# Kernel optimization log

Hardware: AMD Instinct MI355X
Metric: run time of the kernel (lower is better)

## Reference

```python
import jax, jax.numpy as jnp
import numpy as np

N, E, F, C = 100000, 1600000, 64, 256


def setup_inputs() -> dict:
    key = jax.random.key(0)
    ks = jax.random.split(key, 9)

    def lin(k, fi, fo):
        kw, kb = jax.random.split(k)
        w = jax.random.normal(kw, (fi, fo), jnp.float32) * np.float32(1.0 / np.sqrt(fi))
        b = jax.random.normal(kb, (fo,), jnp.float32) * 0.001
        return w, b

    content = jax.random.normal(ks[0], (N, C), jnp.float32)
    node_emb = jax.random.normal(ks[1], (N + 1, F), jnp.float32) * np.float32(1.0 / (100 * F))
    proj_w, proj_b = lin(ks[2], C, F)
    c0w1, c0b1 = lin(ks[3], 2 * F, 4 * F)   # first layer: inp=2F -> 4F
    c0w2, c0b2 = lin(ks[4], 4 * F, F)
    c1w1, c1b1 = lin(ks[5], 3 * F, 6 * F)   # prediction layer: inp=3F -> 6F
    c1w2, c1b2 = lin(ks[6], 6 * F, F)
    nid = jnp.arange(N, dtype=jnp.int32)
    src = jax.random.randint(ks[7], (E,), 0, N, dtype=jnp.int32)
    dst = jax.random.randint(ks[8], (E,), 0, N, dtype=jnp.int32)
    return dict(content=content, node_emb=node_emb, proj_w=proj_w, proj_b=proj_b,
                c0w1=c0w1, c0b1=c0b1, c0w2=c0w2, c0b2=c0b2,
                c1w1=c1w1, c1b1=c1b1, c1w2=c1w2, c1b2=c1b2,
                nid=nid, src=src, dst=dst)


def _l2norm(x):
    # per-node L2 renorm with clamp(min=1e-6) like torch .norm().clamp
    n = jnp.linalg.norm(x, axis=1, keepdims=True)
    return x / jnp.maximum(n, 1e-6)


def _forward(content, node_emb, proj_w, proj_b,
             c0w1, c0b1, c0w2, c0b2, c1w1, c1b1, c1w2, c1b2,
             nid, src, dst):
    n = content.shape[0]
    lrelu = lambda x: jax.nn.leaky_relu(x, 0.1)
    # node init: embedding + projected content (GaussianNoise is identity in eval)
    h = node_emb[nid + 1] + lrelu(content @ proj_w + proj_b)
    # w = sum of 'one' over in-neighbors = in-degree
    deg = jax.ops.segment_sum(jnp.ones(src.shape[0], h.dtype), dst, num_segments=n)
    wden = jnp.maximum(deg - 1.0, 1.0)[:, None]  # (w - 1).clamp(min=1)

    # ---- layer 0 (first_layer) ----
    h_agg = jax.ops.segment_sum(h[src], dst, num_segments=n)  # copy_src('h') + sum
    h_agg = (h_agg - h) / wden
    z = lrelu(jnp.concatenate([h, h_agg], axis=1) @ c0w1 + c0b1)
    h_new = _l2norm(lrelu(z @ c0w2 + c0b2))
    h_res = _l2norm(h_agg)  # skip is None since in_dims == out_dims
    h = h_new

    # ---- layer 1 (prediction_layer) ----
    h_agg = jax.ops.segment_sum(h[src], dst, num_segments=n)
    h_res_sum = jax.ops.segment_sum(h_res[src], dst, num_segments=n)
    h_agg = (h_agg - h) / wden
    z = lrelu(jnp.concatenate([h, h_agg, h_res_sum], axis=1) @ c1w1 + c1b1)
    h_new = z @ c1w2 + c1b2  # prediction layer: no trailing LeakyReLU
    return _l2norm(h_new)


def reference(content, node_emb, proj_w, proj_b, c0w1, c0b1, c0w2, c0b2,
              c1w1, c1b1, c1w2, c1b2, nid, src, dst):
    return _forward(content, node_emb, proj_w, proj_b,
                    c0w1, c0b1, c0w2, c0b2, c1w1, c1b1, c1w2, c1b2,
                    nid, src, dst)
```

## Files before the change

### kernel.cpp

```cpp
#include <hip/hip_runtime.h>

typedef _Float16 half_t;
typedef half_t h8 __attribute__((ext_vector_type(8)));
typedef float f32x4 __attribute__((ext_vector_type(4)));
typedef unsigned int uint;

__device__ __forceinline__ float lrelu_f(float x){ return x >= 0.f ? x : 0.1f*x; }

__device__ __forceinline__ float2 unpack_h2(uint v){
  half_t lo = __builtin_bit_cast(half_t, (unsigned short)(v & 0xffffu));
  half_t hi = __builtin_bit_cast(half_t, (unsigned short)(v >> 16));
  return make_float2((float)lo, (float)hi);
}
__device__ __forceinline__ uint pack_h2(float a, float b){
  unsigned short lo = __builtin_bit_cast(unsigned short, (half_t)a);
  unsigned short hi = __builtin_bit_cast(unsigned short, (half_t)b);
  return (uint)lo | ((uint)hi << 16);
}

enum { EPI_INIT=0, EPI_LRELU=1, EPI_LRELU_L2=2, EPI_L2=3 };
constexpr int CAP = 64;

__global__ void pack_all_kernel(const float* __restrict__ s0, half_t* __restrict__ d0,
                                const float* __restrict__ s1, half_t* __restrict__ d1,
                                const float* __restrict__ s2, half_t* __restrict__ d2,
                                const float* __restrict__ s3, half_t* __restrict__ d3,
                                const float* __restrict__ s4, half_t* __restrict__ d4){
  int b = blockIdx.x;
  const float* w; half_t* o; int K, M;
  if      (b < 8)  { w=s0; o=d0; K=256; M=64;  }
  else if (b < 24) { w=s1; o=d1; K=128; M=256; b-=8; }
  else if (b < 32) { w=s2; o=d2; K=256; M=64;  b-=24; }
  else if (b < 68) { w=s3; o=d3; K=192; M=384; b-=32; }
  else             { w=s4; o=d4; K=384; M=64;  b-=68; }
  int idx = b*256 + threadIdx.x;
  int total = (K/32)*(M/16)*64;
  if (idx >= total) return;
  int lane = idx & 63;
  int t = idx >> 6;
  int CBn = M/16;
  int cb = t % CBn;
  int s  = t / CBn;
  int k0 = s*32 + (lane>>4)*8;
  int c  = cb*16 + (lane&15);
  #pragma unroll
  for (int j=0;j<8;++j) o[(size_t)idx*8 + j] = (half_t)w[(size_t)(k0+j)*M + c];
}

template<int IT>
__global__ __launch_bounds__(256) void scatter_kernel(const int* __restrict__ src, const int* __restrict__ dst,
                               int* __restrict__ cnt, int* __restrict__ col, int E, int n){
  int part = blockIdx.x & 7;
  long base = (long)(blockIdx.x >> 3) * (256*IT);
  int lo = (int)((long)n * part / 8);
  int hi = (int)((long)n * (part+1) / 8);
  #pragma unroll
  for (int it=0; it<IT; ++it){
    long i = base + it*256 + threadIdx.x;
    if (i < E){
      int d = __builtin_nontemporal_load(dst + i);
      if (d >= lo && d < hi){
        int s = __builtin_nontemporal_load(src + i);
        int r = atomicAdd(&cnt[d], 1);
        if (r < CAP) col[(size_t)d*CAP + r] = s;
      }
    }
  }
}

template<int K, int MOUT, int EPI>
__global__ __launch_bounds__(256) void gemm_kernel(
  const float* __restrict__ x0, int st0,
  const half_t* __restrict__ wp, const float* __restrict__ bias,
  half_t* __restrict__ outv, int ost,
  const float* __restrict__ emb, const int* __restrict__ nid, int n)
{
  constexpr int KS = K/32;
  constexpr int CB = MOUT/16;
  const int lane = threadIdx.x & 63;
  const int wid  = threadIdx.x >> 6;
  const int row0 = blockIdx.x*64 + wid*16;
  const int arow = row0 + (lane & 15);
  const int arowc = arow < n ? arow : n-1;
  const int khi = (lane>>4)*8;

  f32x4 acc[CB];
  #pragma unroll
  for (int cb=0;cb<CB;++cb) acc[cb] = (f32x4){0.f,0.f,0.f,0.f};

  #pragma unroll
  for (int s=0;s<KS;++s){
    int k0 = s*32 + khi;
    f32x4 a0 = *(const f32x4*)(x0 + (size_t)arowc*st0 + k0);
    f32x4 a1 = *(const f32x4*)(x0 + (size_t)arowc*st0 + k0 + 4);
    h8 af;
    #pragma unroll
    for (int j=0;j<4;++j){ af[j]=(half_t)a0[j]; af[j+4]=(half_t)a1[j]; }
    const h8* wrow = (const h8*)wp + (size_t)(s*CB)*64 + lane;
    #pragma unroll
    for (int cb=0;cb<CB;++cb){
      h8 bf = wrow[cb*64];
      acc[cb] = __builtin_amdgcn_mfma_f32_16x16x32_f16(af, bf, acc[cb], 0,0,0);
    }
  }

  const int cgrp = lane >> 4;
  const int ccol = lane & 15;
  #pragma unroll
  for (int r=0;r<4;++r){
    int R = row0 + cgrp*4 + r;
    int Rc = R < n ? R : n-1;
    if (R < n){
      #pragma unroll
      for (int cb=0;cb<CB;++cb){
        float t = lrelu_f(acc[cb][r] + bias[cb*16+ccol]);
        if constexpr (EPI==EPI_INIT) t += emb[(size_t)(nid[Rc]+1)*64 + cb*16 + ccol];
        outv[(size_t)R*ost + cb*16 + ccol] = (half_t)t;
      }
    }
  }
}

template<int K1, int M1, int M2, int NSRC, int EPI2, bool OUTF16>
__global__ __launch_bounds__(256,4) void mlp_kernel(
  const half_t* __restrict__ x0, const half_t* __restrict__ x1, const half_t* __restrict__ x2,
  int st0, int st1, int st2,
  const half_t* __restrict__ wp1, const float* __restrict__ b1,
  const half_t* __restrict__ wp2, const float* __restrict__ b2,
  void* __restrict__ outv, int ost, int n)
{
  constexpr int RS  = 17;
  constexpr int KS1 = K1/32, CBT = M1/16, CBW = CBT/4;
  constexpr int KS2 = M1/32, CB2 = M2/16;
  constexpr int RED = 65;
  __shared__ uint  zc[M1*RS];
  __shared__ float red[2*16*RED];

  const int lane = threadIdx.x & 63;
  const int wid  = threadIdx.x >> 6;
  const int row0 = blockIdx.x*32;
  const int khi  = (lane>>4)*8;
  const int ccol = lane & 15;
  const int cgrp = lane >> 4;

  f32x4 acc[2][CBW];
  #pragma unroll
  for (int t=0;t<2;++t)
    #pragma unroll
    for (int cb=0;cb<CBW;++cb) acc[t][cb] = (f32x4){0.f,0.f,0.f,0.f};

  #pragma unroll
  for (int s=0;s<KS1;++s){
    int k0 = s*32 + khi;
    const half_t* p = x0; int st = st0; int koff = k0;
    if constexpr (NSRC>1){
      int isrc = k0 >> 6;
      if constexpr (NSRC>=2){ if (isrc==1){ p=x1; st=st1; } }
      if constexpr (NSRC>=3){ if (isrc==2){ p=x2; st=st2; } }
      koff = k0 & 63;
    }
    h8 af[2];
    #pragma unroll
    for (int t=0;t<2;++t){
      int ar = row0 + t*16 + ccol; if (ar >= n) ar = n-1;
      af[t] = *(const h8*)(p + (size_t)ar*st + koff);
    }
    #pragma unroll
    for (int cb=0;cb<CBW;++cb){
      h8 bf = ((const h8*)wp1)[(size_t)(s*CBT + wid*CBW + cb)*64 + lane];
      #pragma unroll
      for (int t=0;t<2;++t)
        acc[t][cb] = __builtin_amdgcn_mfma_f32_16x16x32_f16(af[t], bf, acc[t][cb], 0,0,0);
    }
  }
  #pragma unroll
  for (int t=0;t<2;++t){
    #pragma unroll
    for (int cb=0;cb<CBW;++cb){
      int col = wid*(CBW*16) + cb*16 + ccol;
      float bb = b1[col];
      float v0 = lrelu_f(acc[t][cb][0]+bb);
      float v1 = lrelu_f(acc[t][cb][1]+bb);
      float v2 = lrelu_f(acc[t][cb][2]+bb);
      float v3 = lrelu_f(acc[t][cb][3]+bb);
      int idx = col*RS + t*8 + cgrp*2;
      zc[idx]   = pack_h2(v0,v1);
      zc[idx+1] = pack_h2(v2,v3);
    }
  }
  __syncthreads();

  const int rt = wid & 1, kh = wid >> 1;
  f32x4 acc2[CB2];
  #pragma unroll
  for (int cb=0;cb<CB2;++cb) acc2[cb] = (f32x4){0.f,0.f,0.f,0.f};
  const uint sel = (lane&1) ? 0x07060302u : 0x05040100u;
  const int rp0 = rt*8 + (ccol>>1);

  #pragma unroll
  for (int si=0;si<KS2/2;++si){
    int s = kh*(KS2/2) + si;
    uint v[8];
    #pragma unroll
    for (int j=0;j<8;++j) v[j] = zc[(s*32 + khi + j)*RS + rp0];
    uint4 u;
    u.x = __builtin_amdgcn_perm(v[1], v[0], sel);
    u.y = __builtin_amdgcn_perm(v[3], v[2], sel);
    u.z = __builtin_amdgcn_perm(v[5], v[4], sel);
    u.w = __builtin_amdgcn_perm(v[7], v[6], sel);
    h8 af2 = __builtin_bit_cast(h8, u);
    #pragma unroll
    for (int cb=0;cb<CB2;++cb){
      h8 bf = ((const h8*)wp2)[(size_t)(s*CB2+cb)*64 + lane];
      acc2[cb] = __builtin_amdgcn_mfma_f32_16x16x32_f16(af2, bf, acc2[cb], 0,0,0);
    }
  }
  if (kh == 1){
    #pragma unroll
    for (int cb=0;cb<CB2;++cb)
      #pragma unroll
      for (int r=0;r<4;++r)
        red[(rt*16 + cgrp*4 + r)*RED + cb*16 + ccol] = acc2[cb][r];
  }
  __syncthreads();
  if (kh == 0){
    #pragma unroll
    for (int r=0;r<4;++r){
      int R = row0 + rt*16 + cgrp*4 + r;
      float vv[CB2];
      #pragma unroll
      for (int cb=0;cb<CB2;++cb){
        float t = acc2[cb][r] + red[(rt*16 + cgrp*4 + r)*RED + cb*16 + ccol] + b2[cb*16+ccol];
        if constexpr (EPI2==EPI_LRELU_L2) t = lrelu_f(t);
        vv[cb] = t;
      }
      float sq = 0.f;
      #pragma unroll
      for (int cb=0;cb<CB2;++cb) sq += vv[cb]*vv[cb];
      sq += __shfl_xor(sq,1); sq += __shfl_xor(sq,2);
      sq += __shfl_xor(sq,4); sq += __shfl_xor(sq,8);
      float inv = 1.f / fmaxf(sqrtf(sq), 1e-6f);
      if (R < n){
        #pragma unroll
        for (int cb=0;cb<CB2;++cb){
          float t = vv[cb]*inv;
          if constexpr (OUTF16)
            ((half_t*)outv)[(size_t)R*ost + cb*16 + ccol] = (half_t)t;
          else
            ((float*)outv)[(size_t)R*ost + cb*16 + ccol] = t;
        }
      }
    }
  }
}

__global__ __launch_bounds__(256) void segsum0_kernel(const uint* __restrict__ hu, const int* __restrict__ cnt,
                               const int* __restrict__ col,
                               uint* __restrict__ hagg, uint* __restrict__ hc, int n){
  int node = blockIdx.x*4 + (threadIdx.x>>6);
  if (node >= n) return;
  int lane = threadIdx.x & 63;
  int g = lane >> 3, l = lane & 7;
  int deg = cnt[node];
  int degc = deg < CAP ? deg : CAP;
  const int* cv = col + (size_t)node*CAP;
  float a[8] = {0,0,0,0,0,0,0,0};
  int j = g;
  for (; j + 8 < degc; j += 16){
    int c0 = cv[j], c1 = cv[j+8];
    uint4 v0 = *(const uint4*)(hu + (size_t)c0*32 + l*4);
    uint4 v1 = *(const uint4*)(hu + (size_t)c1*32 + l*4);
    float2 f0=unpack_h2(v0.x), f1=unpack_h2(v0.y), f2=unpack_h2(v0.z), f3=unpack_h2(v0.w);
    float2 g0=unpack_h2(v1.x), g1=unpack_h2(v1.y), g2=unpack_h2(v1.z), g3=unpack_h2(v1.w);
    a[0]+=f0.x+g0.x; a[1]+=f0.y+g0.y; a[2]+=f1.x+g1.x; a[3]+=f1.y+g1.y;
    a[4]+=f2.x+g2.x; a[5]+=f2.y+g2.y; a[6]+=f3.x+g3.x; a[7]+=f3.y+g3.y;
  }
  if (j < degc){
    int c = cv[j];
    uint4 v = *(const uint4*)(hu + (size_t)c*32 + l*4);
    float2 f0=unpack_h2(v.x), f1=unpack_h2(v.y), f2=unpack_h2(v.z), f3=unpack_h2(v.w);
    a[0]+=f0.x; a[1]+=f0.y; a[2]+=f1.x; a[3]+=f1.y;
    a[4]+=f2.x; a[5]+=f2.y; a[6]+=f3.x; a[7]+=f3.y;
  }
  #pragma unroll
  for (int q=0;q<8;++q){
    a[q] += __shfl_xor(a[q], 8);
    a[q] += __shfl_xor(a[q], 16);
    a[q] += __shfl_xor(a[q], 32);
  }
  uint4 hv4 = *(const uint4*)(hu + (size_t)node*32 + l*4);
  float2 b0=unpack_h2(hv4.x), b1=unpack_h2(hv4.y), b2=unpack_h2(hv4.z), b3=unpack_h2(hv4.w);
  float hv[8] = {b0.x,b0.y,b1.x,b1.y,b2.x,b2.y,b3.x,b3.y};
  float iwd = 1.f / fmaxf((float)deg - 1.f, 1.f);
  float sq = 0.f;
  #pragma unroll
  for (int q=0;q<8;++q){ a[q] = (a[q]-hv[q])*iwd; sq += a[q]*a[q]; }
  sq += __shfl_xor(sq,1); sq += __shfl_xor(sq,2); sq += __shfl_xor(sq,4);
  float inv = 1.f / fmaxf(sqrtf(sq), 1e-6f);
  if (g == 0){
    uint4 oa, oh;
    oa.x = pack_h2(a[0],a[1]); oa.y = pack_h2(a[2],a[3]);
    oa.z = pack_h2(a[4],a[5]); oa.w = pack_h2(a[6],a[7]);
    oh.x = pack_h2(a[0]*inv,a[1]*inv); oh.y = pack_h2(a[2]*inv,a[3]*inv);
    oh.z = pack_h2(a[4]*inv,a[5]*inv); oh.w = pack_h2(a[6]*inv,a[7]*inv);
    *(uint4*)(hagg + (size_t)node*32 + l*4) = oa;
    *(uint4*)(hc + (size_t)node*64 + 32 + l*4) = oh;
  }
}

__global__ __launch_bounds__(256) void segsum1_kernel(const uint* __restrict__ hcu, const int* __restrict__ cnt,
                               const int* __restrict__ col,
                               uint* __restrict__ hagg, uint* __restrict__ hsum, int n){
  int node = blockIdx.x*4 + (threadIdx.x>>6);
  if (node >= n) return;
  int lane = threadIdx.x & 63;
  int g = lane >> 4, l = lane & 15;
  int deg = cnt[node];
  int degc = deg < CAP ? deg : CAP;
  const int* cv = col + (size_t)node*CAP;
  float a[8] = {0,0,0,0,0,0,0,0};
  int j = g;
  for (; j + 4 < degc; j += 8){
    int c0 = cv[j], c1 = cv[j+4];
    uint4 v0 = *(const uint4*)(hcu + (size_t)c0*64 + l*4);
    uint4 v1 = *(const uint4*)(hcu + (size_t)c1*64 + l*4);
    float2 f0=unpack_h2(v0.x), f1=unpack_h2(v0.y), f2=unpack_h2(v0.z), f3=unpack_h2(v0.w);
    float2 g0=unpack_h2(v1.x), g1=unpack_h2(v1.y), g2=unpack_h2(v1.z), g3=unpack_h2(v1.w);
    a[0]+=f0.x+g0.x; a[1]+=f0.y+g0.y; a[2]+=f1.x+g1.x; a[3]+=f1.y+g1.y;
    a[4]+=f2.x+g2.x; a[5]+=f2.y+g2.y; a[6]+=f3.x+g3.x; a[7]+=f3.y+g3.y;
  }
  if (j < degc){
    int c = cv[j];
    uint4 v = *(const uint4*)(hcu + (size_t)c*64 + l*4);
    float2 f0=unpack_h2(v.x), f1=unpack_h2(v.y), f2=unpack_h2(v.z), f3=unpack_h2(v.w);
    a[0]+=f0.x; a[1]+=f0.y; a[2]+=f1.x; a[3]+=f1.y;
    a[4]+=f2.x; a[5]+=f2.y; a[6]+=f3.x; a[7]+=f3.y;
  }
  #pragma unroll
  for (int q=0;q<8;++q){
    a[q] += __shfl_xor(a[q], 16);
    a[q] += __shfl_xor(a[q], 32);
  }
  if (g == 0){
    if (l < 8){
      uint4 hv4 = *(const uint4*)(hcu + (size_t)node*64 + l*4);
      float2 b0=unpack_h2(hv4.x), b1=unpack_h2(hv4.y), b2=unpack_h2(hv4.z), b3=unpack_h2(hv4.w);
      float hv[8] = {b0.x,b0.y,b1.x,b1.y,b2.x,b2.y,b3.x,b3.y};
      float iwd = 1.f / fmaxf((float)deg - 1.f, 1.f);
      uint4 o;
      o.x = pack_h2((a[0]-hv[0])*iwd,(a[1]-hv[1])*iwd);
      o.y = pack_h2((a[2]-hv[2])*iwd,(a[3]-hv[3])*iwd);
      o.z = pack_h2((a[4]-hv[4])*iwd,(a[5]-hv[5])*iwd);
      o.w = pack_h2((a[6]-hv[6])*iwd,(a[7]-hv[7])*iwd);
      *(uint4*)(hagg + (size_t)node*32 + l*4) = o;
    } else {
      uint4 o;
      o.x = pack_h2(a[0],a[1]); o.y = pack_h2(a[2],a[3]);
      o.z = pack_h2(a[4],a[5]); o.w = pack_h2(a[6],a[7]);
      *(uint4*)(hsum + (size_t)node*32 + (l-8)*4) = o;
    }
  }
}

extern "C" void kernel_launch(void* const* d_in, const int* in_sizes, int n_in,
                              void* d_out, int out_size, void* d_ws, size_t ws_size,
                              hipStream_t stream){
  const float* content = (const float*)d_in[0];
  const float* node_emb= (const float*)d_in[1];
  const float* proj_w  = (const float*)d_in[2];
  const float* proj_b  = (const float*)d_in[3];
  const float* c0w1 = (const float*)d_in[4];
  const float* c0b1 = (const float*)d_in[5];
  const float* c0w2 = (const float*)d_in[6];
  const float* c0b2 = (const float*)d_in[7];
  const float* c1w1 = (const float*)d_in[8];
  const float* c1b1 = (const float*)d_in[9];
  const float* c1w2 = (const float*)d_in[10];
  const float* c1b2 = (const float*)d_in[11];
  const int* nid = (const int*)d_in[12];
  const int* src = (const int*)d_in[13];
  const int* dst = (const int*)d_in[14];
  float* out = (float*)d_out;
  const int n = in_sizes[12];
  const int E = in_sizes[13];

  char* ws = (char*)d_ws;
  size_t off = 0;
  auto alloc = [&](size_t bytes)->char*{
    char* p = ws + off;
    off = (off + bytes + 255) & ~(size_t)255;
    return p;
  };
  half_t* h0   = (half_t*)alloc((size_t)n*64*2);
  half_t* hc   = (half_t*)alloc((size_t)n*128*2);
  half_t* hagg0= (half_t*)alloc((size_t)n*64*2);
  half_t* hagg1= (half_t*)alloc((size_t)n*64*2);
  half_t* hsum1= (half_t*)alloc((size_t)n*64*2);
  int* cnt    = (int*)alloc((size_t)n*4);
  int* col    = (int*)alloc((size_t)n*CAP*4);
  half_t* wp0 = (half_t*)alloc((size_t)256*64*2);
  half_t* wp1 = (half_t*)alloc((size_t)128*256*2);
  half_t* wp2 = (half_t*)alloc((size_t)256*64*2);
  half_t* wp3 = (half_t*)alloc((size_t)192*384*2);
  half_t* wp4 = (half_t*)alloc((size_t)384*64*2);

  hipMemsetAsync(cnt, 0, (size_t)n*4, stream);

  pack_all_kernel<<<80,256,0,stream>>>(proj_w, wp0, c0w1, wp1, c0w2, wp2, c1w1, wp3, c1w2, wp4);

  {
    constexpr int IT = 4;
    int chunks = (E + 256*IT - 1)/(256*IT);
    scatter_kernel<IT><<<chunks*8,256,0,stream>>>(src, dst, cnt, col, E, n);
  }

  const int rgrid = (n + 63)/64;
  const int mgrid = (n + 31)/32;

  gemm_kernel<256,64,EPI_INIT><<<rgrid,256,0,stream>>>(
      content, 256, wp0, proj_b, h0, 64, node_emb, nid, n);

  segsum0_kernel<<<(n+3)/4,256,0,stream>>>((const uint*)h0, cnt, col,
                                           (uint*)hagg0, (uint*)hc, n);
  mlp_kernel<128,256,64,2,EPI_LRELU_L2,true><<<mgrid,256,0,stream>>>(
      h0, hagg0, nullptr, 64,64,0, wp1, c0b1, wp2, c0b2, hc, 128, n);

  segsum1_kernel<<<(n+3)/4,256,0,stream>>>((const uint*)hc, cnt, col,
                                           (uint*)hagg1, (uint*)hsum1, n);
  mlp_kernel<192,384,64,3,EPI_L2,false><<<mgrid,256,0,stream>>>(
      hc, hagg1, hsum1, 128,64,64, wp3, c1b1, wp4, c1b2, out, 64, n);
}
```

Baseline: 301.8 us.

## Fuse weight packing, edge scatter and input projection GEMM into one interleaved kernel

Merges the weight-pack kernel, the CSR scatter kernel and the input projection GEMM into one launch, interleaving GEMM blocks among scatter blocks so compute-bound and atomic-bound work share the GPU at the same time. Each GEMM block now packs proj_w into shared memory itself rather than reading a prepacked buffer. The scatter path now loads dst and src four at a time with vector loads. Separately, segsum1 unrolls its neighbour-gather loop to four loads in flight. The cost is redundant per-block weight conversion and a larger, more divergent kernel.

```diff
diff --git a/kernel.cpp b/kernel.cpp
--- a/kernel.cpp
+++ b/kernel.cpp
@@ -4,6 +4,7 @@
 typedef half_t h8 __attribute__((ext_vector_type(8)));
 typedef float f32x4 __attribute__((ext_vector_type(4)));
 typedef unsigned int uint;
+typedef int i4 __attribute__((ext_vector_type(4)));
 
 __device__ __forceinline__ float lrelu_f(float x){ return x >= 0.f ? x : 0.1f*x; }
 
@@ -21,101 +22,115 @@
 enum { EPI_INIT=0, EPI_LRELU=1, EPI_LRELU_L2=2, EPI_L2=3 };
 constexpr int CAP = 64;
 
-__global__ void pack_all_kernel(const float* __restrict__ s0, half_t* __restrict__ d0,
-                                const float* __restrict__ s1, half_t* __restrict__ d1,
-                                const float* __restrict__ s2, half_t* __restrict__ d2,
-                                const float* __restrict__ s3, half_t* __restrict__ d3,
-                                const float* __restrict__ s4, half_t* __restrict__ d4){
+__global__ __launch_bounds__(256) void front_kernel(
+    const float* __restrict__ c0w1, half_t* __restrict__ wp1,
+    const float* __restrict__ c0w2, half_t* __restrict__ wp2,
+    const float* __restrict__ c1w1, half_t* __restrict__ wp3,
+    const float* __restrict__ c1w2, half_t* __restrict__ wp4,
+    const int* __restrict__ src, const int* __restrict__ dst,
+    int* __restrict__ cnt, int* __restrict__ col, int E,
+    const float* __restrict__ content, const float* __restrict__ proj_w,
+    const float* __restrict__ proj_b, const float* __restrict__ node_emb,
+    const int* __restrict__ nid, half_t* __restrict__ h0,
+    int n, int nGemm, int nScatter)
+{
+  __shared__ half_t wp0s[16384];
   int b = blockIdx.x;
-  const float* w; half_t* o; int K, M;
-  if      (b < 8)  { w=s0; o=d0; K=256; M=64;  }
-  else if (b < 24) { w=s1; o=d1; K=128; M=256; b-=8; }
-  else if (b < 32) { w=s2; o=d2; K=256; M=64;  b-=24; }
-  else if (b < 68) { w=s3; o=d3; K=192; M=384; b-=32; }
-  else             { w=s4; o=d4; K=384; M=64;  b-=68; }
-  int idx = b*256 + threadIdx.x;
-  int total = (K/32)*(M/16)*64;
-  if (idx >= total) return;
-  int lane = idx & 63;
-  int t = idx >> 6;
-  int CBn = M/16;
-  int cb = t % CBn;
-  int s  = t / CBn;
-  int k0 = s*32 + (lane>>4)*8;
-  int c  = cb*16 + (lane&15);
-  #pragma unroll
-  for (int j=0;j<8;++j) o[(size_t)idx*8 + j] = (half_t)w[(size_t)(k0+j)*M + c];
-}
-
-template<int IT>
-__global__ __launch_bounds__(256) void scatter_kernel(const int* __restrict__ src, const int* __restrict__ dst,
-                               int* __restrict__ cnt, int* __restrict__ col, int E, int n){
-  int part = blockIdx.x & 7;
-  long base = (long)(blockIdx.x >> 3) * (256*IT);
+
+  if (b < 72){
+    const float* w; half_t* o; int K, M;
+    if      (b < 16) { w=c0w1; o=wp1; K=128; M=256; }
+    else if (b < 24) { w=c0w2; o=wp2; K=256; M=64;  b-=16; }
+    else if (b < 60) { w=c1w1; o=wp3; K=192; M=384; b-=24; }
+    else             { w=c1w2; o=wp4; K=384; M=64;  b-=60; }
+    int idx = b*256 + threadIdx.x;
+    int total = (K/32)*(M/16)*64;
+    if (idx >= total) return;
+    int lane = idx & 63;
+    int t = idx >> 6;
+    int CBn = M/16;
+    int cb = t % CBn;
+    int s  = t / CBn;
+    int k0 = s*32 + (lane>>4)*8;
+    int c  = cb*16 + (lane&15);
+    #pragma unroll
+    for (int j=0;j<8;++j) o[(size_t)idx*8 + j] = (half_t)w[(size_t)(k0+j)*M + c];
+    return;
+  }
+
+  int u = b - 72;
+  int R = (nGemm + nScatter) / nGemm;
+
+  if (u % R == 0 && u / R < nGemm){
+    int gb = u / R;
+    const int lane = threadIdx.x & 63;
+    const int wid  = threadIdx.x >> 6;
+    for (int f = threadIdx.x; f < 2048; f += 256){
+      int fl = f & 63; int q = f >> 6; int cb = q & 3; int s = q >> 2;
+      int k0 = s*32 + (fl>>4)*8; int c = cb*16 + (fl&15);
+      h8 fr;
+      #pragma unroll
+      for (int j=0;j<8;++j) fr[j] = (half_t)proj_w[(size_t)(k0+j)*64 + c];
+      ((h8*)wp0s)[f] = fr;
+    }
+    __syncthreads();
+
+    const int row0 = gb*64 + wid*16;
+    const int arow = row0 + (lane & 15);
+    const int arowc = arow < n ? arow : n-1;
+    const int khi = (lane>>4)*8;
+    f32x4 acc[4];
+    #pragma unroll
+    for (int cb=0;cb<4;++cb) acc[cb] = (f32x4){0.f,0.f,0.f,0.f};
+    #pragma unroll
+    for (int s=0;s<8;++s){
+      int k0 = s*32 + khi;
+      f32x4 a0 = *(const f32x4*)(content + (size_t)arowc*256 + k0);
+      f32x4 a1 = *(const f32x4*)(content + (size_t)arowc*256 + k0 + 4);
+      h8 af;
+      #pragma unroll
+      for (int j=0;j<4;++j){ af[j]=(half_t)a0[j]; af[j+4]=(half_t)a1[j]; }
+      #pragma unroll
+      for (int cb=0;cb<4;++cb){
+        h8 bf = ((const h8*)wp0s)[(s*4+cb)*64 + lane];
+        acc[cb] = __builtin_amdgcn_mfma_f32_16x16x32_f16(af, bf, acc[cb], 0,0,0);
+      }
+    }
+    const int cgrp = lane >> 4;
+    const int ccol = lane & 15;
+    #pragma unroll
+    for (int r=0;r<4;++r){
+      int Rr = row0 + cgrp*4 + r;
+      if (Rr < n){
+        #pragma unroll
+        for (int cb=0;cb<4;++cb){
+          float t = lrelu_f(acc[cb][r] + proj_b[cb*16+ccol]);
+          t += node_emb[(size_t)(nid[Rr]+1)*64 + cb*16 + ccol];
+          h0[(size_t)Rr*64 + cb*16 + ccol] = (half_t)t;
+        }
+      }
+    }
+    return;
+  }
+
+  int sb = (u < R*nGemm) ? (u - u/R - 1) : (u - nGemm);
+  int part = sb & 7;
+  long base = (long)(sb >> 3) * 2048;
   int lo = (int)((long)n * part / 8);
   int hi = (int)((long)n * (part+1) / 8);
   #pragma unroll
-  for (int it=0; it<IT; ++it){
-    long i = base + it*256 + threadIdx.x;
-    if (i < E){
-      int d = __builtin_nontemporal_load(dst + i);
-      if (d >= lo && d < hi){
-        int s = __builtin_nontemporal_load(src + i);
-        int r = atomicAdd(&cnt[d], 1);
-        if (r < CAP) col[(size_t)d*CAP + r] = s;
-      }
-    }
-  }
-}
-
-template<int K, int MOUT, int EPI>
-__global__ __launch_bounds__(256) void gemm_kernel(
-  const float* __restrict__ x0, int st0,
-  const half_t* __restrict__ wp, const float* __restrict__ bias,
-  half_t* __restrict__ outv, int ost,
-  const float* __restrict__ emb, const int* __restrict__ nid, int n)
-{
-  constexpr int KS = K/32;
-  constexpr int CB = MOUT/16;
-  const int lane = threadIdx.x & 63;
-  const int wid  = threadIdx.x >> 6;
-  const int row0 = blockIdx.x*64 + wid*16;
-  const int arow = row0 + (lane & 15);
-  const int arowc = arow < n ? arow : n-1;
-  const int khi = (lane>>4)*8;
-
-  f32x4 acc[CB];
-  #pragma unroll
-  for (int cb=0;cb<CB;++cb) acc[cb] = (f32x4){0.f,0.f,0.f,0.f};
-
-  #pragma unroll
-  for (int s=0;s<KS;++s){
-    int k0 = s*32 + khi;
-    f32x4 a0 = *(const f32x4*)(x0 + (size_t)arowc*st0 + k0);
-    f32x4 a1 = *(const f32x4*)(x0 + (size_t)arowc*st0 + k0 + 4);
-    h8 af;
-    #pragma unroll
-    for (int j=0;j<4;++j){ af[j]=(half_t)a0[j]; af[j+4]=(half_t)a1[j]; }
-    const h8* wrow = (const h8*)wp + (size_t)(s*CB)*64 + lane;
-    #pragma unroll
-    for (int cb=0;cb<CB;++cb){
-      h8 bf = wrow[cb*64];
-      acc[cb] = __builtin_amdgcn_mfma_f32_16x16x32_f16(af, bf, acc[cb], 0,0,0);
-    }
-  }
-
-  const int cgrp = lane >> 4;
-  const int ccol = lane & 15;
-  #pragma unroll
-  for (int r=0;r<4;++r){
-    int R = row0 + cgrp*4 + r;
-    int Rc = R < n ? R : n-1;
-    if (R < n){
-      #pragma unroll
-      for (int cb=0;cb<CB;++cb){
-        float t = lrelu_f(acc[cb][r] + bias[cb*16+ccol]);
-        if constexpr (EPI==EPI_INIT) t += emb[(size_t)(nid[Rc]+1)*64 + cb*16 + ccol];
-        outv[(size_t)R*ost + cb*16 + ccol] = (half_t)t;
+  for (int half = 0; half < 2; ++half){
+    long i0 = base + half*1024 + threadIdx.x*4;
+    if (i0 < E){
+      i4 d4 = __builtin_nontemporal_load((const i4*)(dst + i0));
+      bool m0 = d4.x>=lo && d4.x<hi, m1 = d4.y>=lo && d4.y<hi;
+      bool m2 = d4.z>=lo && d4.z<hi, m3 = d4.w>=lo && d4.w<hi;
+      if (m0|m1|m2|m3){
+        i4 s4 = __builtin_nontemporal_load((const i4*)(src + i0));
+        if (m0){ int r = atomicAdd(&cnt[d4.x],1); if (r<CAP) col[(size_t)d4.x*CAP+r] = s4.x; }
+        if (m1){ int r = atomicAdd(&cnt[d4.y],1); if (r<CAP) col[(size_t)d4.y*CAP+r] = s4.y; }
+        if (m2){ int r = atomicAdd(&cnt[d4.z],1); if (r<CAP) col[(size_t)d4.z*CAP+r] = s4.z; }
+        if (m3){ int r = atomicAdd(&cnt[d4.w],1); if (r<CAP) col[(size_t)d4.w*CAP+r] = s4.w; }
       }
     }
   }
@@ -226,7 +241,7 @@
   if (kh == 0){
     #pragma unroll
     for (int r=0;r<4;++r){
-      int R = row0 + rt*16 + cgrp*4 + r;
+      int Rr = row0 + rt*16 + cgrp*4 + r;
       float vv[CB2];
       #pragma unroll
       for (int cb=0;cb<CB2;++cb){
@@ -240,14 +255,14 @@
       sq += __shfl_xor(sq,1); sq += __shfl_xor(sq,2);
       sq += __shfl_xor(sq,4); sq += __shfl_xor(sq,8);
       float inv = 1.f / fmaxf(sqrtf(sq), 1e-6f);
-      if (R < n){
+      if (Rr < n){
         #pragma unroll
         for (int cb=0;cb<CB2;++cb){
           float t = vv[cb]*inv;
           if constexpr (OUTF16)
-            ((half_t*)outv)[(size_t)R*ost + cb*16 + ccol] = (half_t)t;
+            ((half_t*)outv)[(size_t)Rr*ost + cb*16 + ccol] = (half_t)t;
           else
-            ((float*)outv)[(size_t)R*ost + cb*16 + ccol] = t;
+            ((float*)outv)[(size_t)Rr*ost + cb*16 + ccol] = t;
         }
       }
     }
@@ -320,16 +335,23 @@
   const int* cv = col + (size_t)node*CAP;
   float a[8] = {0,0,0,0,0,0,0,0};
   int j = g;
-  for (; j + 4 < degc; j += 8){
-    int c0 = cv[j], c1 = cv[j+4];
+  for (; j + 12 < degc; j += 16){
+    int c0 = cv[j], c1 = cv[j+4], c2 = cv[j+8], c3 = cv[j+12];
     uint4 v0 = *(const uint4*)(hcu + (size_t)c0*64 + l*4);
     uint4 v1 = *(const uint4*)(hcu + (size_t)c1*64 + l*4);
-    float2 f0=unpack_h2(v0.x), f1=unpack_h2(v0.y), f2=unpack_h2(v0.z), f3=unpack_h2(v0.w);
-    float2 g0=unpack_h2(v1.x), g1=unpack_h2(v1.y), g2=unpack_h2(v1.z), g3=unpack_h2(v1.w);
-    a[0]+=f0.x+g0.x; a[1]+=f0.y+g0.y; a[2]+=f1.x+g1.x; a[3]+=f1.y+g1.y;
-    a[4]+=f2.x+g2.x; a[5]+=f2.y+g2.y; a[6]+=f3.x+g3.x; a[7]+=f3.y+g3.y;
-  }
-  if (j < degc){
+    uint4 v2 = *(const uint4*)(hcu + (size_t)c2*64 + l*4);
+    uint4 v3 = *(const uint4*)(hcu + (size_t)c3*64 + l*4);
+    float2 e0, e1, e2, e3;
+    e0=unpack_h2(v0.x); e1=unpack_h2(v0.y); e2=unpack_h2(v0.z); e3=unpack_h2(v0.w);
+    a[0]+=e0.x; a[1]+=e0.y; a[2]+=e1.x; a[3]+=e1.y; a[4]+=e2.x; a[5]+=e2.y; a[6]+=e3.x; a[7]+=e3.y;
+    e0=unpack_h2(v1.x); e1=unpack_h2(v1.y); e2=unpack_h2(v1.z); e3=unpack_h2(v1.w);
+    a[0]+=e0.x; a[1]+=e0.y; a[2]+=e1.x; a[3]+=e1.y; a[4]+=e2.x; a[5]+=e2.y; a[6]+=e3.x; a[7]+=e3.y;
+    e0=unpack_h2(v2.x); e1=unpack_h2(v2.y); e2=unpack_h2(v2.z); e3=unpack_h2(v2.w);
+    a[0]+=e0.x; a[1]+=e0.y; a[2]+=e1.x; a[3]+=e1.y; a[4]+=e2.x; a[5]+=e2.y; a[6]+=e3.x; a[7]+=e3.y;
+    e0=unpack_h2(v3.x); e1=unpack_h2(v3.y); e2=unpack_h2(v3.z); e3=unpack_h2(v3.w);
+    a[0]+=e0.x; a[1]+=e0.y; a[2]+=e1.x; a[3]+=e1.y; a[4]+=e2.x; a[5]+=e2.y; a[6]+=e3.x; a[7]+=e3.y;
+  }
+  for (; j < degc; j += 4){
     int c = cv[j];
     uint4 v = *(const uint4*)(hcu + (size_t)c*64 + l*4);
     float2 f0=unpack_h2(v.x), f1=unpack_h2(v.y), f2=unpack_h2(v.z), f3=unpack_h2(v.w);
@@ -398,7 +420,6 @@
   half_t* hsum1= (half_t*)alloc((size_t)n*64*2);
   int* cnt    = (int*)alloc((size_t)n*4);
   int* col    = (int*)alloc((size_t)n*CAP*4);
-  half_t* wp0 = (half_t*)alloc((size_t)256*64*2);
   half_t* wp1 = (half_t*)alloc((size_t)128*256*2);
   half_t* wp2 = (half_t*)alloc((size_t)256*64*2);
   half_t* wp3 = (half_t*)alloc((size_t)192*384*2);
@@ -406,19 +427,15 @@
 
   hipMemsetAsync(cnt, 0, (size_t)n*4, stream);
 
-  pack_all_kernel<<<80,256,0,stream>>>(proj_w, wp0, c0w1, wp1, c0w2, wp2, c1w1, wp3, c1w2, wp4);
-
-  {
-    constexpr int IT = 4;
-    int chunks = (E + 256*IT - 1)/(256*IT);
-    scatter_kernel<IT><<<chunks*8,256,0,stream>>>(src, dst, cnt, col, E, n);
-  }
-
-  const int rgrid = (n + 63)/64;
+  const int nGemm = (n + 63)/64;
+  const int nScatter = ((E + 2047)/2048)*8;
+  front_kernel<<<72 + nGemm + nScatter, 256, 0, stream>>>(
+      c0w1, wp1, c0w2, wp2, c1w1, wp3, c1w2, wp4,
+      src, dst, cnt, col, E,
+      content, proj_w, proj_b, node_emb, nid, h0,
+      n, nGemm, nScatter);
+
   const int mgrid = (n + 31)/32;
-
-  gemm_kernel<256,64,EPI_INIT><<<rgrid,256,0,stream>>>(
-      content, 256, wp0, proj_b, h0, 64, node_emb, nid, n);
 
   segsum0_kernel<<<(n+3)/4,256,0,stream>>>((const uint*)h0, cnt, col,
                                            (uint*)hagg0, (uint*)hc, n);
```

New measurement: 312.1 us. 1.03x slower.

## Replace filtered multi-pass edge scatter with two-phase binning through staging buffer

Applied to the files above, without the earlier changes.

The old scatter had each of 8 node partitions re-read the full dst array and keep only its own edges, which read the edge list eight times. The new code reads each edge once, bins it into one of 8 node-range buckets per chunk using shared-memory counters, and writes (dst,src) pairs to a staging buffer. A second kernel then replays each bucket and does the atomic insertion into the CSR-like column table. The segsum1 gather loop is also unrolled to issue 4 neighbor loads per iteration. The cost is extra staging writes and reads, plus silent edge drops if a bucket exceeds SLOT; with 2048 edges per chunk the expected bucket size is about 256, so overflow is unlikely.

```diff
diff --git a/kernel.cpp b/kernel.cpp
--- a/kernel.cpp
+++ b/kernel.cpp
@@ -4,6 +4,7 @@
 typedef half_t h8 __attribute__((ext_vector_type(8)));
 typedef float f32x4 __attribute__((ext_vector_type(4)));
 typedef unsigned int uint;
+typedef unsigned long long ull;
 
 __device__ __forceinline__ float lrelu_f(float x){ return x >= 0.f ? x : 0.1f*x; }
 
@@ -20,6 +21,7 @@
 
 enum { EPI_INIT=0, EPI_LRELU=1, EPI_LRELU_L2=2, EPI_L2=3 };
 constexpr int CAP = 64;
+constexpr int SLOT = 768;
 
 __global__ void pack_all_kernel(const float* __restrict__ s0, half_t* __restrict__ d0,
                                 const float* __restrict__ s1, half_t* __restrict__ d1,
@@ -48,23 +50,43 @@
 }
 
 template<int IT>
-__global__ __launch_bounds__(256) void scatter_kernel(const int* __restrict__ src, const int* __restrict__ dst,
-                               int* __restrict__ cnt, int* __restrict__ col, int E, int n){
-  int part = blockIdx.x & 7;
-  long base = (long)(blockIdx.x >> 3) * (256*IT);
-  int lo = (int)((long)n * part / 8);
-  int hi = (int)((long)n * (part+1) / 8);
+__global__ __launch_bounds__(256) void binA_kernel(const int* __restrict__ src, const int* __restrict__ dst,
+    ull* __restrict__ staging, int* __restrict__ cntsPC, int E, int n){
+  __shared__ int lcnt[8];
+  if (threadIdx.x < 8) lcnt[threadIdx.x] = 0;
+  __syncthreads();
+  int chunk = blockIdx.x;
+  long base = (long)chunk * (256*IT);
   #pragma unroll
   for (int it=0; it<IT; ++it){
     long i = base + it*256 + threadIdx.x;
     if (i < E){
       int d = __builtin_nontemporal_load(dst + i);
-      if (d >= lo && d < hi){
-        int s = __builtin_nontemporal_load(src + i);
-        int r = atomicAdd(&cnt[d], 1);
-        if (r < CAP) col[(size_t)d*CAP + r] = s;
-      }
-    }
+      int s = __builtin_nontemporal_load(src + i);
+      int p = (int)(((long)d*8)/n);
+      int pos = atomicAdd(&lcnt[p], 1);
+      if (pos < SLOT)
+        staging[((size_t)chunk*8 + p)*SLOT + pos] = ((ull)(uint)d << 32) | (uint)s;
+    }
+  }
+  __syncthreads();
+  if (threadIdx.x < 8){
+    int c = lcnt[threadIdx.x];
+    cntsPC[chunk*8 + threadIdx.x] = c < SLOT ? c : SLOT;
+  }
+}
+
+__global__ __launch_bounds__(256) void scatB_kernel(const ull* __restrict__ staging,
+    const int* __restrict__ cntsPC, int* __restrict__ cnt, int* __restrict__ col){
+  int b = blockIdx.x;
+  int c = cntsPC[b];
+  const ull* sp = staging + (size_t)b*SLOT;
+  for (int j = threadIdx.x; j < c; j += 256){
+    ull v = __builtin_nontemporal_load(sp + j);
+    int d = (int)(v >> 32);
+    int s = (int)(v & 0xffffffffu);
+    int r = atomicAdd(&cnt[d], 1);
+    if (r < CAP) col[(size_t)d*CAP + r] = s;
   }
 }
 
@@ -109,12 +131,11 @@
   #pragma unroll
   for (int r=0;r<4;++r){
     int R = row0 + cgrp*4 + r;
-    int Rc = R < n ? R : n-1;
     if (R < n){
       #pragma unroll
       for (int cb=0;cb<CB;++cb){
         float t = lrelu_f(acc[cb][r] + bias[cb*16+ccol]);
-        if constexpr (EPI==EPI_INIT) t += emb[(size_t)(nid[Rc]+1)*64 + cb*16 + ccol];
+        if constexpr (EPI==EPI_INIT) t += emb[(size_t)(nid[R]+1)*64 + cb*16 + ccol];
         outv[(size_t)R*ost + cb*16 + ccol] = (half_t)t;
       }
     }
@@ -226,7 +247,7 @@
   if (kh == 0){
     #pragma unroll
     for (int r=0;r<4;++r){
-      int R = row0 + rt*16 + cgrp*4 + r;
+      int Rr = row0 + rt*16 + cgrp*4 + r;
       float vv[CB2];
       #pragma unroll
       for (int cb=0;cb<CB2;++cb){
@@ -240,14 +261,14 @@
       sq += __shfl_xor(sq,1); sq += __shfl_xor(sq,2);
       sq += __shfl_xor(sq,4); sq += __shfl_xor(sq,8);
       float inv = 1.f / fmaxf(sqrtf(sq), 1e-6f);
-      if (R < n){
+      if (Rr < n){
         #pragma unroll
         for (int cb=0;cb<CB2;++cb){
           float t = vv[cb]*inv;
           if constexpr (OUTF16)
-            ((half_t*)outv)[(size_t)R*ost + cb*16 + ccol] = (half_t)t;
+            ((half_t*)outv)[(size_t)Rr*ost + cb*16 + ccol] = (half_t)t;
           else
-            ((float*)outv)[(size_t)R*ost + cb*16 + ccol] = t;
+            ((float*)outv)[(size_t)Rr*ost + cb*16 + ccol] = t;
         }
       }
     }
@@ -320,16 +341,23 @@
   const int* cv = col + (size_t)node*CAP;
   float a[8] = {0,0,0,0,0,0,0,0};
   int j = g;
-  for (; j + 4 < degc; j += 8){
-    int c0 = cv[j], c1 = cv[j+4];
+  for (; j + 12 < degc; j += 16){
+    int c0 = cv[j], c1 = cv[j+4], c2 = cv[j+8], c3 = cv[j+12];
     uint4 v0 = *(const uint4*)(hcu + (size_t)c0*64 + l*4);
     uint4 v1 = *(const uint4*)(hcu + (size_t)c1*64 + l*4);
-    float2 f0=unpack_h2(v0.x), f1=unpack_h2(v0.y), f2=unpack_h2(v0.z), f3=unpack_h2(v0.w);
-    float2 g0=unpack_h2(v1.x), g1=unpack_h2(v1.y), g2=unpack_h2(v1.z), g3=unpack_h2(v1.w);
-    a[0]+=f0.x+g0.x; a[1]+=f0.y+g0.y; a[2]+=f1.x+g1.x; a[3]+=f1.y+g1.y;
-    a[4]+=f2.x+g2.x; a[5]+=f2.y+g2.y; a[6]+=f3.x+g3.x; a[7]+=f3.y+g3.y;
-  }
-  if (j < degc){
+    uint4 v2 = *(const uint4*)(hcu + (size_t)c2*64 + l*4);
+    uint4 v3 = *(const uint4*)(hcu + (size_t)c3*64 + l*4);
+    float2 e0, e1, e2, e3;
+    e0=unpack_h2(v0.x); e1=unpack_h2(v0.y); e2=unpack_h2(v0.z); e3=unpack_h2(v0.w);
+    a[0]+=e0.x; a[1]+=e0.y; a[2]+=e1.x; a[3]+=e1.y; a[4]+=e2.x; a[5]+=e2.y; a[6]+=e3.x; a[7]+=e3.y;
+    e0=unpack_h2(v1.x); e1=unpack_h2(v1.y); e2=unpack_h2(v1.z); e3=unpack_h2(v1.w);
+    a[0]+=e0.x; a[1]+=e0.y; a[2]+=e1.x; a[3]+=e1.y; a[4]+=e2.x; a[5]+=e2.y; a[6]+=e3.x; a[7]+=e3.y;
+    e0=unpack_h2(v2.x); e1=unpack_h2(v2.y); e2=unpack_h2(v2.z); e3=unpack_h2(v2.w);
+    a[0]+=e0.x; a[1]+=e0.y; a[2]+=e1.x; a[3]+=e1.y; a[4]+=e2.x; a[5]+=e2.y; a[6]+=e3.x; a[7]+=e3.y;
+    e0=unpack_h2(v3.x); e1=unpack_h2(v3.y); e2=unpack_h2(v3.z); e3=unpack_h2(v3.w);
+    a[0]+=e0.x; a[1]+=e0.y; a[2]+=e1.x; a[3]+=e1.y; a[4]+=e2.x; a[5]+=e2.y; a[6]+=e3.x; a[7]+=e3.y;
+  }
+  for (; j < degc; j += 4){
     int c = cv[j];
     uint4 v = *(const uint4*)(hcu + (size_t)c*64 + l*4);
     float2 f0=unpack_h2(v.x), f1=unpack_h2(v.y), f2=unpack_h2(v.z), f3=unpack_h2(v.w);
@@ -391,6 +419,7 @@
     off = (off + bytes + 255) & ~(size_t)255;
     return p;
   };
+  const int nChunks = (E + 2047)/2048;
   half_t* h0   = (half_t*)alloc((size_t)n*64*2);
   half_t* hc   = (half_t*)alloc((size_t)n*128*2);
   half_t* hagg0= (half_t*)alloc((size_t)n*64*2);
@@ -398,6 +427,8 @@
   half_t* hsum1= (half_t*)alloc((size_t)n*64*2);
   int* cnt    = (int*)alloc((size_t)n*4);
   int* col    = (int*)alloc((size_t)n*CAP*4);
+  ull* staging= (ull*)alloc((size_t)nChunks*8*SLOT*8);
+  int* cntsPC = (int*)alloc((size_t)nChunks*8*4);
   half_t* wp0 = (half_t*)alloc((size_t)256*64*2);
   half_t* wp1 = (half_t*)alloc((size_t)128*256*2);
   half_t* wp2 = (half_t*)alloc((size_t)256*64*2);
@@ -408,11 +439,8 @@
 
   pack_all_kernel<<<80,256,0,stream>>>(proj_w, wp0, c0w1, wp1, c0w2, wp2, c1w1, wp3, c1w2, wp4);
 
-  {
-    constexpr int IT = 4;
-    int chunks = (E + 256*IT - 1)/(256*IT);
-    scatter_kernel<IT><<<chunks*8,256,0,stream>>>(src, dst, cnt, col, E, n);
-  }
+  binA_kernel<8><<<nChunks,256,0,stream>>>(src, dst, staging, cntsPC, E, n);
+  scatB_kernel<<<nChunks*8,256,0,stream>>>(staging, cntsPC, cnt, col);
 
   const int rgrid = (n + 63)/64;
   const int mgrid = (n + 31)/32;
```

Result: no change. 301.7 us (-0.0%).
